# Optimization experiments

Hardware: AMD Instinct MI355X
Metric: run time of the kernel (lower is better)

Reference implementation:

```python
import jax, jax.numpy as jnp
import numpy as np

B, S, D, H = 2, 2048, 1024, 16
HD = D // H  # 64


def setup_inputs() -> dict:
    key = jax.random.key(0)
    ks = jax.random.split(key, 7)
    std = 1.0 / np.sqrt(D)
    return {
        "q": jax.random.normal(ks[0], (B, S, D), jnp.float32),
        "k": jax.random.normal(ks[1], (B, S, D), jnp.float32),
        "v": jax.random.normal(ks[2], (B, S, D), jnp.float32),
        "w_q": jax.random.normal(ks[3], (D, D), jnp.float32) * std,
        "w_k": jax.random.normal(ks[4], (D, D), jnp.float32) * std,
        "w_v": jax.random.normal(ks[5], (D, D), jnp.float32) * std,
        "w_o": jax.random.normal(ks[6], (D, D), jnp.float32) * std,
    }


def reference(q, k, v, w_q, w_k, w_v, w_o):
    # Linear (torch nn.Linear, no bias): y = x @ W.T
    Q = jnp.einsum('bsd,ed->bse', q, w_q)
    K = jnp.einsum('bsd,ed->bse', k, w_k)
    V = jnp.einsum('bsd,ed->bse', v, w_v)
    # split heads -> (B, H, S, HD)
    Qh = Q.reshape(B, S, H, HD).transpose(0, 2, 1, 3)
    Kh = K.reshape(B, S, H, HD).transpose(0, 2, 1, 3)
    Vh = V.reshape(B, S, H, HD).transpose(0, 2, 1, 3)
    scale = 1.0 / np.sqrt(HD).astype(np.float32)
    scores = jnp.einsum('bhqd,bhkd->bhqk', Qh, Kh) * scale  # [B,H,S,S]
    attn = jax.nn.softmax(scores, axis=-1)
    ctx = jnp.einsum('bhqk,bhkd->bhqd', attn, Vh)
    combined = ctx.transpose(0, 2, 1, 3).reshape(B, S, D)
    out = jnp.einsum('bsd,ed->bse', combined, w_o)
    return out, attn
```

## Files before the change

kernel.cpp:

```cpp
#include <hip/hip_runtime.h>
#include <hip/hip_bf16.h>
#include <cstdint>

#define B_ 2
#define S_ 2048
#define D_ 1024
#define H_ 16
#define HD_ 64

#define SCALE_LOG2 0.18033688011112042f

typedef __attribute__((ext_vector_type(8))) __bf16 bf16x8;
typedef __attribute__((ext_vector_type(8))) unsigned short ushort8;
typedef __attribute__((ext_vector_type(4))) unsigned short ushort4v;
typedef __attribute__((ext_vector_type(4))) float f32x4;
typedef __attribute__((ext_vector_type(16))) float f32x16;

__device__ __forceinline__ unsigned short f2bf(float f) {
  __bf16 h = (__bf16)f;
  return __builtin_bit_cast(unsigned short, h);
}

__device__ __forceinline__ float bf2f(unsigned short u) {
  union { unsigned int i; float f; } v; v.i = ((unsigned int)u) << 16; return v.f;
}

__device__ __forceinline__ float fexp2(float x) {
#if __has_builtin(__builtin_amdgcn_exp2f)
  return __builtin_amdgcn_exp2f(x);
#else
  return exp2f(x);
#endif
}

__device__ __forceinline__ f32x4 mfma16(bf16x8 a, bf16x8 b, f32x4 c) {
  return __builtin_amdgcn_mfma_f32_16x16x32_bf16(a, b, c, 0, 0, 0);
}
__device__ __forceinline__ f32x16 mfma32(bf16x8 a, bf16x8 b, f32x16 c) {
  return __builtin_amdgcn_mfma_f32_32x32x16_bf16(a, b, c, 0, 0, 0);
}

#define LGKM_BARRIER()                                        \
  do {                                                        \
    asm volatile("s_waitcnt lgkmcnt(0)" ::: "memory");        \
    __builtin_amdgcn_s_barrier();                             \
  } while (0)

__global__ __launch_bounds__(256) void proj_qkv_kernel(
    const float* __restrict__ qin, const float* __restrict__ kin,
    const float* __restrict__ vin, const float* __restrict__ wq,
    const float* __restrict__ wk, const float* __restrict__ wv,
    unsigned short* __restrict__ qh, unsigned short* __restrict__ kh,
    unsigned short* __restrict__ vt)
{
  __shared__ unsigned short As[128][40];
  __shared__ unsigned short Bs[128][40];

  const int z = blockIdx.z;
  const float* X = (z == 0) ? qin : (z == 1) ? kin : vin;
  const float* W = (z == 0) ? wq : (z == 1) ? wk : wv;
  unsigned short* dst = (z == 0) ? qh : (z == 1) ? kh : vt;
  const float osc = (z == 0) ? SCALE_LOG2 : 1.0f;

  const int lin = blockIdx.x + 8 * blockIdx.y;
  const int swz = (lin & 7) * 32 + (lin >> 3);
  const int bx = swz & 7, by = swz >> 3;

  const int tid = threadIdx.x;
  const int lane = tid & 63, wid = tid >> 6;
  const int c = lane & 15, g = lane >> 4;
  const int wr = wid >> 1, wc = wid & 1;
  const int m0 = by * 128, n0 = bx * 128;

  const int sr = tid >> 1, sh = tid & 1;
  const float* Ap = X + (size_t)(m0 + sr) * D_ + sh * 16;
  const float* Bp = W + (size_t)(n0 + sr) * D_ + sh * 16;

  float ar[16], br[16];
  f32x4 acc[4][4];
#pragma unroll
  for (int i = 0; i < 4; ++i)
#pragma unroll
    for (int j = 0; j < 4; ++j) acc[i][j] = (f32x4){0.f, 0.f, 0.f, 0.f};

  auto ldg_tile = [&](int kt) {
    const float* ap = Ap + kt * 32;
    const float* bp = Bp + kt * 32;
#pragma unroll
    for (int j = 0; j < 4; ++j) {
      *(f32x4*)(ar + 4 * j) = *(const f32x4*)(ap + 4 * j);
      *(f32x4*)(br + 4 * j) = *(const f32x4*)(bp + 4 * j);
    }
  };
  auto sts_tile = [&]() {
    unsigned short ta[16], tb[16];
#pragma unroll
    for (int j = 0; j < 16; ++j) { ta[j] = f2bf(ar[j]); tb[j] = f2bf(br[j]); }
    *(ushort8*)&As[sr][sh * 16]     = *(ushort8*)&ta[0];
    *(ushort8*)&As[sr][sh * 16 + 8] = *(ushort8*)&ta[8];
    *(ushort8*)&Bs[sr][sh * 16]     = *(ushort8*)&tb[0];
    *(ushort8*)&Bs[sr][sh * 16 + 8] = *(ushort8*)&tb[8];
  };

  ldg_tile(0);
  sts_tile();
  __syncthreads();

  for (int kt = 0; kt < 32; ++kt) {
    if (kt < 31) ldg_tile(kt + 1);
    bf16x8 af[4], bfr[4];
#pragma unroll
    for (int i = 0; i < 4; ++i) af[i]  = *(bf16x8*)&As[wr * 64 + i * 16 + c][g * 8];
#pragma unroll
    for (int i = 0; i < 4; ++i) bfr[i] = *(bf16x8*)&Bs[wc * 64 + i * 16 + c][g * 8];
#pragma unroll
    for (int mi = 0; mi < 4; ++mi)
#pragma unroll
      for (int ni = 0; ni < 4; ++ni)
        acc[mi][ni] = mfma16(af[mi], bfr[ni], acc[mi][ni]);
    __syncthreads();
    if (kt < 31) { sts_tile(); __syncthreads(); }
  }

#pragma unroll
  for (int mi = 0; mi < 4; ++mi) {
#pragma unroll
    for (int ni = 0; ni < 4; ++ni) {
      const int n = n0 + wc * 64 + ni * 16 + c;
      const int h = n >> 6, hd = n & 63;
      if (z < 2) {
#pragma unroll
        for (int r = 0; r < 4; ++r) {
          const int m = m0 + wr * 64 + mi * 16 + g * 4 + r;
          const int b = m >> 11, s = m & 2047;
          dst[((size_t)(b * H_ + h) * S_ + s) * HD_ + hd] = f2bf(acc[mi][ni][r] * osc);
        }
      } else {
        const int m = m0 + wr * 64 + mi * 16 + g * 4;
        const int b = m >> 11, s = m & 2047;
        ushort4v pk;
#pragma unroll
        for (int r = 0; r < 4; ++r) pk[r] = f2bf(acc[mi][ni][r]);
        *(ushort4v*)&dst[((size_t)(b * H_ + h) * HD_ + hd) * S_ + s] = pk;
      }
    }
  }
}

__global__ __launch_bounds__(256) void attn_kernel(
    const unsigned short* __restrict__ qh, const unsigned short* __restrict__ kh,
    const unsigned short* __restrict__ vt, float* __restrict__ attn,
    unsigned short* __restrict__ comb)
{
  __shared__ unsigned short Ks[64][72];
  __shared__ unsigned short Vs[64][72];
  __shared__ unsigned short Ps[4][32][72];

  const int tid = threadIdx.x;
  const int lane = tid & 63, w = tid >> 6;
  const int q32 = lane & 31, hi = lane >> 5;
  const int c = lane & 15, g = lane >> 4;

  const int lin = blockIdx.x;
  const int swz = (lin & 7) * 64 + (lin >> 3);
  const int bh = swz >> 4;
  const int q0 = (swz & 15) * 128;
  const int qw = q0 + w * 32;

  const unsigned short* Qb = qh + (size_t)bh * S_ * HD_;
  const unsigned short* Kb = kh + (size_t)bh * S_ * HD_;
  const unsigned short* Vb = vt + (size_t)bh * HD_ * S_;
  float* attnb = attn + (size_t)bh * S_ * S_;

  const int sr = tid >> 2;
  const int scol = (tid & 3) * 16;

  bf16x8 aQ[4];
#pragma unroll
  for (int t = 0; t < 4; ++t)
    aQ[t] = *(const bf16x8*)(Qb + (size_t)(qw + q32) * HD_ + t * 16 + hi * 8);

  const unsigned short* Kst = Kb + (size_t)sr * HD_ + scol;
  const unsigned short* Vst = Vb + (size_t)sr * S_ + scol;

  float l4[4] = {0.f, 0.f, 0.f, 0.f};
  ushort8 kr0 = *(const ushort8*)Kst;
  ushort8 kr1 = *(const ushort8*)(Kst + 8);

  for (int kt = 0; kt < 32; ++kt) {
    *(ushort8*)&Ks[sr][scol]     = kr0;
    *(ushort8*)&Ks[sr][scol + 8] = kr1;
    LGKM_BARRIER();
    if (kt < 31) {
      const unsigned short* p = Kst + (size_t)(kt + 1) * 64 * HD_;
      kr0 = *(const ushort8*)p;
      kr1 = *(const ushort8*)(p + 8);
    }
#pragma unroll
    for (int kb = 0; kb < 2; ++kb) {
      f32x16 p = (f32x16)(0.f);
#pragma unroll
      for (int t = 0; t < 4; ++t)
        p = mfma32(*(bf16x8*)&Ks[kb * 32 + q32][t * 16 + hi * 8], aQ[t], p);
#pragma unroll
      for (int r = 0; r < 16; ++r) l4[r & 3] += fexp2(p[r]);
    }
    LGKM_BARRIER();
  }
  float l = (l4[0] + l4[1]) + (l4[2] + l4[3]);
  l += __shfl_xor(l, 32);
  const float invl = 1.f / l;

  f32x16 ctx0 = (f32x16)(0.f), ctx1 = (f32x16)(0.f);

  float* srow = attnb + (size_t)(qw + g) * S_ + c * 4;

  kr0 = *(const ushort8*)Kst;
  kr1 = *(const ushort8*)(Kst + 8);
  ushort8 vr0 = *(const ushort8*)Vst;
  ushort8 vr1 = *(const ushort8*)(Vst + 8);

  for (int kt = 0; kt < 32; ++kt) {
    *(ushort8*)&Ks[sr][scol]     = kr0;
    *(ushort8*)&Ks[sr][scol + 8] = kr1;
    *(ushort8*)&Vs[sr][scol]     = vr0;
    *(ushort8*)&Vs[sr][scol + 8] = vr1;
    LGKM_BARRIER();
    if (kt < 31) {
      const unsigned short* p = Kst + (size_t)(kt + 1) * 64 * HD_;
      const unsigned short* q = Vst + (kt + 1) * 64;
      kr0 = *(const ushort8*)p;
      kr1 = *(const ushort8*)(p + 8);
      vr0 = *(const ushort8*)q;
      vr1 = *(const ushort8*)(q + 8);
    }

#pragma unroll
    for (int kb = 0; kb < 2; ++kb) {
      f32x16 p = (f32x16)(0.f);
#pragma unroll
      for (int t = 0; t < 4; ++t)
        p = mfma32(*(bf16x8*)&Ks[kb * 32 + q32][t * 16 + hi * 8], aQ[t], p);
#pragma unroll
      for (int j = 0; j < 4; ++j) {
        ushort4v pk;
#pragma unroll
        for (int r = 0; r < 4; ++r) pk[r] = f2bf(fexp2(p[4 * j + r]) * invl);
        *(ushort4v*)&Ps[w][q32][kb * 32 + 8 * j + 4 * hi] = pk;
      }
    }

    bf16x8 pa[4];
#pragma unroll
    for (int t = 0; t < 4; ++t)
      pa[t] = *(bf16x8*)&Ps[w][q32][t * 16 + hi * 8];
#pragma unroll
    for (int t = 0; t < 4; ++t) {
      ctx0 = mfma32(pa[t], *(bf16x8*)&Vs[q32][t * 16 + hi * 8],      ctx0);
      ctx1 = mfma32(pa[t], *(bf16x8*)&Vs[32 + q32][t * 16 + hi * 8], ctx1);
    }

#pragma unroll
    for (int it = 0; it < 8; ++it) {
      ushort4v pb = *(ushort4v*)&Ps[w][it * 4 + g][c * 4];
      f32x4 pf;
#pragma unroll
      for (int r = 0; r < 4; ++r) pf[r] = bf2f(pb[r]);
      __builtin_nontemporal_store(pf, (f32x4*)(srow + (size_t)it * 4 * S_ + kt * 64));
    }
    LGKM_BARRIER();
  }

  const int b = bh >> 4, h = bh & 15;
#pragma unroll
  for (int r = 0; r < 16; ++r) {
    const int qrow = (r & 3) + 8 * (r >> 2) + 4 * hi;
    unsigned short* cb = comb + (size_t)(b * S_ + qw + qrow) * D_ + h * 64 + q32;
    cb[0]  = f2bf(ctx0[r]);
    cb[32] = f2bf(ctx1[r]);
  }
}

__global__ __launch_bounds__(256) void out_proj_kernel(
    const unsigned short* __restrict__ comb, const float* __restrict__ wo,
    float* __restrict__ out)
{
  __shared__ unsigned short As[128][40];
  __shared__ unsigned short Bs[128][40];

  const int lin = blockIdx.x + 8 * blockIdx.y;
  const int swz = (lin & 7) * 32 + (lin >> 3);
  const int bx = swz & 7, by = swz >> 3;

  const int tid = threadIdx.x;
  const int lane = tid & 63, wid = tid >> 6;
  const int c = lane & 15, g = lane >> 4;
  const int wr = wid >> 1, wc = wid & 1;
  const int m0 = by * 128, n0 = bx * 128;
  const int sr = tid >> 1, sh = tid & 1;

  const unsigned short* Apb = comb + (size_t)(m0 + sr) * D_ + sh * 16;
  const float* Bpb = wo + (size_t)(n0 + sr) * D_ + sh * 16;

  ushort8 ar2[2];
  float br[16];
  f32x4 acc[4][4];
#pragma unroll
  for (int i = 0; i < 4; ++i)
#pragma unroll
    for (int j = 0; j < 4; ++j) acc[i][j] = (f32x4){0.f, 0.f, 0.f, 0.f};

  auto ldg_tile = [&](int kt) {
    ar2[0] = *(const ushort8*)(Apb + kt * 32);
    ar2[1] = *(const ushort8*)(Apb + kt * 32 + 8);
#pragma unroll
    for (int j = 0; j < 4; ++j)
      *(f32x4*)(br + 4 * j) = *(const f32x4*)(Bpb + kt * 32 + 4 * j);
  };
  auto sts_tile = [&]() {
    *(ushort8*)&As[sr][sh * 16]     = ar2[0];
    *(ushort8*)&As[sr][sh * 16 + 8] = ar2[1];
    unsigned short tb[16];
#pragma unroll
    for (int j = 0; j < 16; ++j) tb[j] = f2bf(br[j]);
    *(ushort8*)&Bs[sr][sh * 16]     = *(ushort8*)&tb[0];
    *(ushort8*)&Bs[sr][sh * 16 + 8] = *(ushort8*)&tb[8];
  };

  ldg_tile(0);
  sts_tile();
  __syncthreads();

  for (int kt = 0; kt < 32; ++kt) {
    if (kt < 31) ldg_tile(kt + 1);
    bf16x8 af[4], bfr[4];
#pragma unroll
    for (int i = 0; i < 4; ++i) af[i]  = *(bf16x8*)&As[wr * 64 + i * 16 + c][g * 8];
#pragma unroll
    for (int i = 0; i < 4; ++i) bfr[i] = *(bf16x8*)&Bs[wc * 64 + i * 16 + c][g * 8];
#pragma unroll
    for (int mi = 0; mi < 4; ++mi)
#pragma unroll
      for (int ni = 0; ni < 4; ++ni)
        acc[mi][ni] = mfma16(af[mi], bfr[ni], acc[mi][ni]);
    __syncthreads();
    if (kt < 31) { sts_tile(); __syncthreads(); }
  }

#pragma unroll
  for (int mi = 0; mi < 4; ++mi)
#pragma unroll
    for (int ni = 0; ni < 4; ++ni)
#pragma unroll
      for (int r = 0; r < 4; ++r) {
        const int m = m0 + wr * 64 + mi * 16 + g * 4 + r;
        const int n = n0 + wc * 64 + ni * 16 + c;
        out[(size_t)m * D_ + n] = acc[mi][ni][r];
      }
}

extern "C" void kernel_launch(void* const* d_in, const int* in_sizes, int n_in,
                              void* d_out, int out_size, void* d_ws, size_t ws_size,
                              hipStream_t stream)
{
  const float* q  = (const float*)d_in[0];
  const float* k  = (const float*)d_in[1];
  const float* v  = (const float*)d_in[2];
  const float* wq = (const float*)d_in[3];
  const float* wk = (const float*)d_in[4];
  const float* wv = (const float*)d_in[5];
  const float* wo = (const float*)d_in[6];

  float* out  = (float*)d_out;
  float* attn = out + (size_t)B_ * S_ * D_;

  const size_t NE = (size_t)B_ * S_ * D_;
  unsigned short* qh   = (unsigned short*)d_ws;
  unsigned short* kh   = qh + NE;
  unsigned short* vt   = kh + NE;
  unsigned short* comb = vt + NE;

  proj_qkv_kernel<<<dim3(8, 32, 3), dim3(256), 0, stream>>>(q, k, v, wq, wk, wv, qh, kh, vt);
  attn_kernel<<<dim3(512), dim3(256), 0, stream>>>(qh, kh, vt, attn, comb);
  out_proj_kernel<<<dim3(8, 32), dim3(256), 0, stream>>>(comb, wo, out);
}
```

Before: 234.1 us.

## Double-buffer K/V tiles and halve attention block size to two waves

The attention kernel now double-buffers its K and V shared-memory tiles by iteration parity. This drops the trailing barrier in each loop iteration, so global loads and LDS stores for the next tile can overlap compute on the current one. Blocks shrink from four waves to two (64 query rows each), with the grid doubled to 1024 and the block-index swizzle adjusted to match. The aim is less synchronization stall and better occupancy and latency hiding, at the cost of reloading K/V from global memory twice as often per query row.

```diff
diff --git a/kernel.cpp b/kernel.cpp
--- a/kernel.cpp
+++ b/kernel.cpp
@@ -147,14 +147,14 @@
   }
 }
 
-__global__ __launch_bounds__(256) void attn_kernel(
+__global__ __launch_bounds__(128) void attn_kernel(
     const unsigned short* __restrict__ qh, const unsigned short* __restrict__ kh,
     const unsigned short* __restrict__ vt, float* __restrict__ attn,
     unsigned short* __restrict__ comb)
 {
-  __shared__ unsigned short Ks[64][72];
-  __shared__ unsigned short Vs[64][72];
-  __shared__ unsigned short Ps[4][32][72];
+  __shared__ unsigned short Ks[2][64][72];
+  __shared__ unsigned short Vs[2][64][72];
+  __shared__ unsigned short Ps[2][32][72];
 
   const int tid = threadIdx.x;
   const int lane = tid & 63, w = tid >> 6;
@@ -162,9 +162,9 @@
   const int c = lane & 15, g = lane >> 4;
 
   const int lin = blockIdx.x;
-  const int swz = (lin & 7) * 64 + (lin >> 3);
-  const int bh = swz >> 4;
-  const int q0 = (swz & 15) * 128;
+  const int swz = (lin & 7) * 128 + (lin >> 3);
+  const int bh = swz >> 5;
+  const int q0 = (swz & 31) * 64;
   const int qw = q0 + w * 32;
 
   const unsigned short* Qb = qh + (size_t)bh * S_ * HD_;
@@ -172,40 +172,42 @@
   const unsigned short* Vb = vt + (size_t)bh * HD_ * S_;
   float* attnb = attn + (size_t)bh * S_ * S_;
 
-  const int sr = tid >> 2;
-  const int scol = (tid & 3) * 16;
+  const int sr = tid >> 1;
+  const int scb = (tid & 1) * 32;
 
   bf16x8 aQ[4];
 #pragma unroll
   for (int t = 0; t < 4; ++t)
     aQ[t] = *(const bf16x8*)(Qb + (size_t)(qw + q32) * HD_ + t * 16 + hi * 8);
 
-  const unsigned short* Kst = Kb + (size_t)sr * HD_ + scol;
-  const unsigned short* Vst = Vb + (size_t)sr * S_ + scol;
+  const unsigned short* Kst = Kb + (size_t)sr * HD_ + scb;
+  const unsigned short* Vst = Vb + (size_t)sr * S_ + scb;
 
   float l4[4] = {0.f, 0.f, 0.f, 0.f};
-  ushort8 kr0 = *(const ushort8*)Kst;
-  ushort8 kr1 = *(const ushort8*)(Kst + 8);
-
-  for (int kt = 0; kt < 32; ++kt) {
-    *(ushort8*)&Ks[sr][scol]     = kr0;
-    *(ushort8*)&Ks[sr][scol + 8] = kr1;
-    LGKM_BARRIER();
-    if (kt < 31) {
-      const unsigned short* p = Kst + (size_t)(kt + 1) * 64 * HD_;
-      kr0 = *(const ushort8*)p;
-      kr1 = *(const ushort8*)(p + 8);
-    }
-#pragma unroll
-    for (int kb = 0; kb < 2; ++kb) {
-      f32x16 p = (f32x16)(0.f);
-#pragma unroll
-      for (int t = 0; t < 4; ++t)
-        p = mfma32(*(bf16x8*)&Ks[kb * 32 + q32][t * 16 + hi * 8], aQ[t], p);
-#pragma unroll
-      for (int r = 0; r < 16; ++r) l4[r & 3] += fexp2(p[r]);
-    }
-    LGKM_BARRIER();
+  {
+    ushort8 kr[4];
+#pragma unroll
+    for (int j = 0; j < 4; ++j) kr[j] = *(const ushort8*)(Kst + j * 8);
+    for (int kt = 0; kt < 32; ++kt) {
+      const int p = kt & 1;
+#pragma unroll
+      for (int j = 0; j < 4; ++j) *(ushort8*)&Ks[p][sr][scb + j * 8] = kr[j];
+      if (kt < 31) {
+        const unsigned short* np = Kst + (size_t)(kt + 1) * 64 * HD_;
+#pragma unroll
+        for (int j = 0; j < 4; ++j) kr[j] = *(const ushort8*)(np + j * 8);
+      }
+      LGKM_BARRIER();
+#pragma unroll
+      for (int kb = 0; kb < 2; ++kb) {
+        f32x16 pm = (f32x16)(0.f);
+#pragma unroll
+        for (int t = 0; t < 4; ++t)
+          pm = mfma32(*(bf16x8*)&Ks[p][kb * 32 + q32][t * 16 + hi * 8], aQ[t], pm);
+#pragma unroll
+        for (int r = 0; r < 16; ++r) l4[r & 3] += fexp2(pm[r]);
+      }
+    }
   }
   float l = (l4[0] + l4[1]) + (l4[2] + l4[3]);
   l += __shfl_xor(l, 32);
@@ -215,60 +217,65 @@
 
   float* srow = attnb + (size_t)(qw + g) * S_ + c * 4;
 
-  kr0 = *(const ushort8*)Kst;
-  kr1 = *(const ushort8*)(Kst + 8);
-  ushort8 vr0 = *(const ushort8*)Vst;
-  ushort8 vr1 = *(const ushort8*)(Vst + 8);
-
-  for (int kt = 0; kt < 32; ++kt) {
-    *(ushort8*)&Ks[sr][scol]     = kr0;
-    *(ushort8*)&Ks[sr][scol + 8] = kr1;
-    *(ushort8*)&Vs[sr][scol]     = vr0;
-    *(ushort8*)&Vs[sr][scol + 8] = vr1;
-    LGKM_BARRIER();
-    if (kt < 31) {
-      const unsigned short* p = Kst + (size_t)(kt + 1) * 64 * HD_;
-      const unsigned short* q = Vst + (kt + 1) * 64;
-      kr0 = *(const ushort8*)p;
-      kr1 = *(const ushort8*)(p + 8);
-      vr0 = *(const ushort8*)q;
-      vr1 = *(const ushort8*)(q + 8);
-    }
-
-#pragma unroll
-    for (int kb = 0; kb < 2; ++kb) {
-      f32x16 p = (f32x16)(0.f);
+  {
+    ushort8 kr[4], vr[4];
+#pragma unroll
+    for (int j = 0; j < 4; ++j) {
+      kr[j] = *(const ushort8*)(Kst + j * 8);
+      vr[j] = *(const ushort8*)(Vst + j * 8);
+    }
+    for (int kt = 0; kt < 32; ++kt) {
+      const int p = kt & 1;
+#pragma unroll
+      for (int j = 0; j < 4; ++j) {
+        *(ushort8*)&Ks[p][sr][scb + j * 8] = kr[j];
+        *(ushort8*)&Vs[p][sr][scb + j * 8] = vr[j];
+      }
+      if (kt < 31) {
+        const unsigned short* np = Kst + (size_t)(kt + 1) * 64 * HD_;
+        const unsigned short* nq = Vst + (kt + 1) * 64;
+#pragma unroll
+        for (int j = 0; j < 4; ++j) {
+          kr[j] = *(const ushort8*)(np + j * 8);
+          vr[j] = *(const ushort8*)(nq + j * 8);
+        }
+      }
+      LGKM_BARRIER();
+
+#pragma unroll
+      for (int kb = 0; kb < 2; ++kb) {
+        f32x16 pm = (f32x16)(0.f);
+#pragma unroll
+        for (int t = 0; t < 4; ++t)
+          pm = mfma32(*(bf16x8*)&Ks[p][kb * 32 + q32][t * 16 + hi * 8], aQ[t], pm);
+#pragma unroll
+        for (int j = 0; j < 4; ++j) {
+          ushort4v pk;
+#pragma unroll
+          for (int r = 0; r < 4; ++r) pk[r] = f2bf(fexp2(pm[4 * j + r]) * invl);
+          *(ushort4v*)&Ps[w][q32][kb * 32 + 8 * j + 4 * hi] = pk;
+        }
+      }
+
+      bf16x8 pa[4];
 #pragma unroll
       for (int t = 0; t < 4; ++t)
-        p = mfma32(*(bf16x8*)&Ks[kb * 32 + q32][t * 16 + hi * 8], aQ[t], p);
-#pragma unroll
-      for (int j = 0; j < 4; ++j) {
-        ushort4v pk;
-#pragma unroll
-        for (int r = 0; r < 4; ++r) pk[r] = f2bf(fexp2(p[4 * j + r]) * invl);
-        *(ushort4v*)&Ps[w][q32][kb * 32 + 8 * j + 4 * hi] = pk;
-      }
-    }
-
-    bf16x8 pa[4];
-#pragma unroll
-    for (int t = 0; t < 4; ++t)
-      pa[t] = *(bf16x8*)&Ps[w][q32][t * 16 + hi * 8];
-#pragma unroll
-    for (int t = 0; t < 4; ++t) {
-      ctx0 = mfma32(pa[t], *(bf16x8*)&Vs[q32][t * 16 + hi * 8],      ctx0);
-      ctx1 = mfma32(pa[t], *(bf16x8*)&Vs[32 + q32][t * 16 + hi * 8], ctx1);
-    }
-
-#pragma unroll
-    for (int it = 0; it < 8; ++it) {
-      ushort4v pb = *(ushort4v*)&Ps[w][it * 4 + g][c * 4];
-      f32x4 pf;
-#pragma unroll
-      for (int r = 0; r < 4; ++r) pf[r] = bf2f(pb[r]);
-      __builtin_nontemporal_store(pf, (f32x4*)(srow + (size_t)it * 4 * S_ + kt * 64));
-    }
-    LGKM_BARRIER();
+        pa[t] = *(bf16x8*)&Ps[w][q32][t * 16 + hi * 8];
+#pragma unroll
+      for (int t = 0; t < 4; ++t) {
+        ctx0 = mfma32(pa[t], *(bf16x8*)&Vs[p][q32][t * 16 + hi * 8],      ctx0);
+        ctx1 = mfma32(pa[t], *(bf16x8*)&Vs[p][32 + q32][t * 16 + hi * 8], ctx1);
+      }
+
+#pragma unroll
+      for (int it = 0; it < 8; ++it) {
+        ushort4v pb = *(ushort4v*)&Ps[w][it * 4 + g][c * 4];
+        f32x4 pf;
+#pragma unroll
+        for (int r = 0; r < 4; ++r) pf[r] = bf2f(pb[r]);
+        __builtin_nontemporal_store(pf, (f32x4*)(srow + (size_t)it * 4 * S_ + kt * 64));
+      }
+    }
   }
 
   const int b = bh >> 4, h = bh & 15;
@@ -381,6 +388,6 @@
   unsigned short* comb = vt + NE;
 
   proj_qkv_kernel<<<dim3(8, 32, 3), dim3(256), 0, stream>>>(q, k, v, wq, wk, wv, qh, kh, vt);
-  attn_kernel<<<dim3(512), dim3(256), 0, stream>>>(qh, kh, vt, attn, comb);
+  attn_kernel<<<dim3(1024), dim3(128), 0, stream>>>(qh, kh, vt, attn, comb);
   out_proj_kernel<<<dim3(8, 32), dim3(256), 0, stream>>>(comb, wo, out);
 }
```

New measurement: 244.7 us. 4.5% more time.
